# Kernel optimization log

Hardware: AMD Instinct MI355X
Metric: run time of the kernel (lower is better)

Reference implementation:

```python
import jax, jax.numpy as jnp
import numpy as np
from jax import lax

PAD0, PAD1 = 2, 2  # kernel_size=3 -> pad = (3//2+1, (3+1)//2) = (2, 2)


def make_blur_kernel():
    k = jnp.array([1.0, 3.0, 3.0, 1.0], dtype=jnp.float32)
    k2 = k[None, :] * k[:, None]  # [4,4] binomial
    return k2 / jnp.sum(k2)


def setup_inputs() -> dict:
    key = jax.random.key(0)
    x = jax.random.normal(key, (16, 256, 128, 128), dtype=jnp.float32)
    kernel = make_blur_kernel()  # fixed (buffer) 4x4 normalized binomial filter
    return {"x": x, "kernel": kernel}


def reference(x, kernel):
    # upfirdn2d(x, k, up=1, down=1, padding=(2,2)):
    # zero-pad H and W by (2,2) each, depthwise FIR filter with the 4x4 kernel.
    # Kernel is symmetric, so correlation == convolution.
    C = x.shape[1]
    w = jnp.broadcast_to(kernel[None, None, :, :], (C, 1, 4, 4))  # depthwise OIHW
    out = lax.conv_general_dilated(
        x, w,
        window_strides=(1, 1),
        padding=((PAD0, PAD1), (PAD0, PAD1)),
        feature_group_count=C,
        dimension_numbers=("NCHW", "OIHW", "NCHW"),
    )
    # output: [16, 256, 129, 129] (H + pad0 + pad1 - 4 + 1)
    return out
```

## Files before the change

### kernel.cpp

```cpp
#include <hip/hip_runtime.h>


#define BAR() __builtin_amdgcn_s_barrier()
#define WAITV(NSTR) do {                                                     \
        asm volatile("s_waitcnt vmcnt(" NSTR ")" ::: "memory");              \
        __builtin_amdgcn_sched_barrier(0);                                   \
    } while (0)

__global__ __launch_bounds__(512, 8) void blur_fir_ring4(
    const float* __restrict__ x,
    const float* __restrict__ kern,
    float* __restrict__ out)
{
    __shared__ __align__(16) float lds[4 * 16 * 128];

    const int tid  = threadIdx.x;
    const int wv   = tid >> 6;
    const int lane = tid & 63;
    const int c    = tid >> 5;
    const int g    = tid & 31;
    const bool lv  = (g >= 1);

    const float* __restrict__ xi = x + (size_t)blockIdx.x * (128 * 128);
    float* __restrict__ oi = out + (size_t)blockIdx.x * (129 * 129);

    float w[4][4];
#pragma unroll
    for (int p = 0; p < 4; ++p)
#pragma unroll
        for (int q = 0; q < 4; ++q)
            w[p][q] = kern[4 * p + q];

#define STAGE(J) do {                                                        \
        int p0_ = 16 * (J) - 2 + 2 * wv;                                     \
        p0_ = p0_ < 0 ? 0 : (p0_ > 126 ? 126 : p0_);      \
        const float* src_ = xi + (size_t)p0_ * 128 + (lane << 2);            \
        const float* dst_ = &lds[((J) & 3) * 2048 + wv * 256];               \
        __builtin_amdgcn_global_load_lds(                                    \
            (const __attribute__((address_space(1))) unsigned int*)src_,     \
            (__attribute__((address_space(3))) unsigned int*)dst_,           \
            16, 0, 0);                                                       \
    } while (0)

#define COMPUTE(J) do {                                                      \
        float o0 = 0.f, o1 = 0.f, o2 = 0.f, o3 = 0.f;                        \
        float e0 = 0.f, e1 = 0.f, e2 = 0.f;                                  \
        _Pragma("unroll")                                                    \
        for (int p = 0; p < 4; ++p) {                                        \
            const int  k_   = c + p;                                         \
            const bool okr_ = ((unsigned)(16 * (J) - 2 + k_)) < 128u;        \
            const float* pb_ = ((k_ < 16)                                    \
                ? &lds[((J) & 3) * 2048 + k_ * 128]                          \
                : &lds[(((J) + 1) & 3) * 2048 + (k_ - 16) * 128])            \
                + 4 * g - 4;                                                 \
            float4 a_ = make_float4(0.f, 0.f, 0.f, 0.f);                     \
            float4 b_ = make_float4(0.f, 0.f, 0.f, 0.f);                     \
            if (okr_ && lv) a_ = *(const float4*)pb_;                        \
            if (okr_)       b_ = *(const float4*)(pb_ + 4);                  \
            o0 = fmaf(a_.x, w[p][0], o0);                                    \
            o1 = fmaf(a_.y, w[p][0], o1);                                    \
            o2 = fmaf(a_.z, w[p][0], o2);                                    \
            o3 = fmaf(a_.w, w[p][0], o3);                                    \
            o0 = fmaf(a_.y, w[p][1], o0);                                    \
            o1 = fmaf(a_.z, w[p][1], o1);                                    \
            o2 = fmaf(a_.w, w[p][1], o2);                                    \
            o3 = fmaf(b_.x, w[p][1], o3);                                    \
            o0 = fmaf(a_.z, w[p][2], o0);                                    \
            o1 = fmaf(a_.w, w[p][2], o1);                                    \
            o2 = fmaf(b_.x, w[p][2], o2);                                    \
            o3 = fmaf(b_.y, w[p][2], o3);                                    \
            o0 = fmaf(a_.w, w[p][3], o0);                                    \
            o1 = fmaf(b_.x, w[p][3], o1);                                    \
            o2 = fmaf(b_.y, w[p][3], o2);                                    \
            o3 = fmaf(b_.z, w[p][3], o3);                                    \
               \
            e0 = fmaf(b_.x, w[p][0], e0);                                    \
            e0 = fmaf(b_.y, w[p][1], e0);                                    \
            e0 = fmaf(b_.z, w[p][2], e0);                                    \
            e0 = fmaf(b_.w, w[p][3], e0);                                    \
            e1 = fmaf(b_.y, w[p][0], e1);                                    \
            e1 = fmaf(b_.z, w[p][1], e1);                                    \
            e1 = fmaf(b_.w, w[p][2], e1);                                    \
            e2 = fmaf(b_.z, w[p][0], e2);                                    \
            e2 = fmaf(b_.w, w[p][1], e2);                                    \
        }                                                                    \
        float* po_ = oi + (size_t)(16 * (J) + c) * 129 + 4 * g - 2;          \
        if (lv) { po_[0] = o0; po_[1] = o1; }                                \
        po_[2] = o2;                                                         \
        po_[3] = o3;                                                         \
        if (g == 31) { po_[4] = e0; po_[5] = e1; po_[6] = e2; }              \
    } while (0)

    STAGE(0); STAGE(1); STAGE(2); STAGE(3);

    WAITV("2");  BAR(); COMPUTE(0); BAR(); STAGE(4);
    WAITV("9");  BAR(); COMPUTE(1); BAR(); STAGE(5);
    WAITV("16"); BAR(); COMPUTE(2); BAR(); STAGE(6);
    WAITV("16"); BAR(); COMPUTE(3); BAR(); STAGE(7);
    WAITV("16"); BAR(); COMPUTE(4); BAR(); STAGE(8);
    WAITV("16"); BAR(); COMPUTE(5); BAR();
    WAITV("15"); BAR(); COMPUTE(6); BAR();
    WAITV("14"); BAR(); COMPUTE(7); BAR();

    if (c == 0) COMPUTE(8);

#undef STAGE
#undef COMPUTE
}

extern "C" void kernel_launch(void* const* d_in, const int* in_sizes, int n_in,
                              void* d_out, int out_size, void* d_ws, size_t ws_size,
                              hipStream_t stream) {
    const float* x    = (const float*)d_in[0];
    const float* kern = (const float*)d_in[1];
    float* out        = (float*)d_out;

    dim3 grid(4096), block(512);
    hipLaunchKernelGGL(blur_fir_ring4, grid, block, 0, stream, x, kern, out);
}
```

Baseline: 116.0 us.

## Give each wave a private LDS ring to drop block barriers; split right-edge columns into separate kernel

Each wave now stages and consumes only its own 16-row band through a private 6-slot LDS ring. This removes the block-wide s_barrier calls between stages, using only vmcnt/lgkmcnt waits. Each thread computes two output rows per iteration, reusing the loaded input rows for both. The three rightmost output columns, formerly handled by a divergent g==31 branch, move to a second small kernel, which adds a launch and some redundant global reads. LDS use grows and the occupancy hint drops from 8 to 6 blocks.

```diff
diff --git a/kernel.cpp b/kernel.cpp
--- a/kernel.cpp
+++ b/kernel.cpp
@@ -1,25 +1,28 @@
 #include <hip/hip_runtime.h>
 
 
-#define BAR() __builtin_amdgcn_s_barrier()
 #define WAITV(NSTR) do {                                                     \
         asm volatile("s_waitcnt vmcnt(" NSTR ")" ::: "memory");              \
         __builtin_amdgcn_sched_barrier(0);                                   \
     } while (0)
+#define WAITL() do {                                                         \
+        asm volatile("s_waitcnt lgkmcnt(0)" ::: "memory");                   \
+        __builtin_amdgcn_sched_barrier(0);                                   \
+    } while (0)
 
-__global__ __launch_bounds__(512, 8) void blur_fir_ring4(
+__global__ __launch_bounds__(512, 6) void blur_main(
     const float* __restrict__ x,
     const float* __restrict__ kern,
     float* __restrict__ out)
 {
-    __shared__ __align__(16) float lds[4 * 16 * 128];
+    __shared__ __align__(16) float lds[8 * 6 * 256];
 
     const int tid  = threadIdx.x;
     const int wv   = tid >> 6;
     const int lane = tid & 63;
-    const int c    = tid >> 5;
-    const int g    = tid & 31;
-    const bool lv  = (g >= 1);
+    const int h    = lane >> 5;
+    const int g    = lane & 31;
+    const int r0   = wv << 4;
 
     const float* __restrict__ xi = x + (size_t)blockIdx.x * (128 * 128);
     float* __restrict__ oi = out + (size_t)blockIdx.x * (129 * 129);
@@ -31,81 +34,136 @@
         for (int q = 0; q < 4; ++q)
             w[p][q] = kern[4 * p + q];
 
-#define STAGE(J) do {                                                        \
-        int p0_ = 16 * (J) - 2 + 2 * wv;                                     \
-        p0_ = p0_ < 0 ? 0 : (p0_ > 126 ? 126 : p0_);      \
+    float* const wbase = &lds[wv * 1536];
+
+#define STAGEPAIR(Q) do {                                                    \
+        int p0_ = r0 - 2 + 2 * (Q);                                          \
+        p0_ = p0_ < 0 ? 0 : (p0_ > 126 ? 126 : p0_);                         \
         const float* src_ = xi + (size_t)p0_ * 128 + (lane << 2);            \
-        const float* dst_ = &lds[((J) & 3) * 2048 + wv * 256];               \
+        const float* dst_ = wbase + ((Q) % 6) * 256;                         \
         __builtin_amdgcn_global_load_lds(                                    \
             (const __attribute__((address_space(1))) unsigned int*)src_,     \
             (__attribute__((address_space(3))) unsigned int*)dst_,           \
             16, 0, 0);                                                       \
     } while (0)
 
-#define COMPUTE(J) do {                                                      \
-        float o0 = 0.f, o1 = 0.f, o2 = 0.f, o3 = 0.f;                        \
-        float e0 = 0.f, e1 = 0.f, e2 = 0.f;                                  \
-        _Pragma("unroll")                                                    \
-        for (int p = 0; p < 4; ++p) {                                        \
-            const int  k_   = c + p;                                         \
-            const bool okr_ = ((unsigned)(16 * (J) - 2 + k_)) < 128u;        \
-            const float* pb_ = ((k_ < 16)                                    \
-                ? &lds[((J) & 3) * 2048 + k_ * 128]                          \
-                : &lds[(((J) + 1) & 3) * 2048 + (k_ - 16) * 128])            \
-                + 4 * g - 4;                                                 \
-            float4 a_ = make_float4(0.f, 0.f, 0.f, 0.f);                     \
-            float4 b_ = make_float4(0.f, 0.f, 0.f, 0.f);                     \
-            if (okr_ && lv) a_ = *(const float4*)pb_;                        \
-            if (okr_)       b_ = *(const float4*)(pb_ + 4);                  \
-            o0 = fmaf(a_.x, w[p][0], o0);                                    \
-            o1 = fmaf(a_.y, w[p][0], o1);                                    \
-            o2 = fmaf(a_.z, w[p][0], o2);                                    \
-            o3 = fmaf(a_.w, w[p][0], o3);                                    \
-            o0 = fmaf(a_.y, w[p][1], o0);                                    \
-            o1 = fmaf(a_.z, w[p][1], o1);                                    \
-            o2 = fmaf(a_.w, w[p][1], o2);                                    \
-            o3 = fmaf(b_.x, w[p][1], o3);                                    \
-            o0 = fmaf(a_.z, w[p][2], o0);                                    \
-            o1 = fmaf(a_.w, w[p][2], o1);                                    \
-            o2 = fmaf(b_.x, w[p][2], o2);                                    \
-            o3 = fmaf(b_.y, w[p][2], o3);                                    \
-            o0 = fmaf(a_.w, w[p][3], o0);                                    \
-            o1 = fmaf(b_.x, w[p][3], o1);                                    \
-            o2 = fmaf(b_.y, w[p][3], o2);                                    \
-            o3 = fmaf(b_.z, w[p][3], o3);                                    \
-               \
-            e0 = fmaf(b_.x, w[p][0], e0);                                    \
-            e0 = fmaf(b_.y, w[p][1], e0);                                    \
-            e0 = fmaf(b_.z, w[p][2], e0);                                    \
-            e0 = fmaf(b_.w, w[p][3], e0);                                    \
-            e1 = fmaf(b_.y, w[p][0], e1);                                    \
-            e1 = fmaf(b_.z, w[p][1], e1);                                    \
-            e1 = fmaf(b_.w, w[p][2], e1);                                    \
-            e2 = fmaf(b_.z, w[p][0], e2);                                    \
-            e2 = fmaf(b_.w, w[p][1], e2);                                    \
-        }                                                                    \
-        float* po_ = oi + (size_t)(16 * (J) + c) * 129 + 4 * g - 2;          \
-        if (lv) { po_[0] = o0; po_[1] = o1; }                                \
-        po_[2] = o2;                                                         \
-        po_[3] = o3;                                                         \
-        if (g == 31) { po_[4] = e0; po_[5] = e1; po_[6] = e2; }              \
+#define FMA4(O0, O1, O2, O3, AV, BV, P) do {                                 \
+        O0 = fmaf(AV.x, w[P][0], O0);                                        \
+        O0 = fmaf(AV.y, w[P][1], O0);                                        \
+        O0 = fmaf(AV.z, w[P][2], O0);                                        \
+        O0 = fmaf(AV.w, w[P][3], O0);                                        \
+        O1 = fmaf(AV.y, w[P][0], O1);                                        \
+        O1 = fmaf(AV.z, w[P][1], O1);                                        \
+        O1 = fmaf(AV.w, w[P][2], O1);                                        \
+        O1 = fmaf(BV.x, w[P][3], O1);                                        \
+        O2 = fmaf(AV.z, w[P][0], O2);                                        \
+        O2 = fmaf(AV.w, w[P][1], O2);                                        \
+        O2 = fmaf(BV.x, w[P][2], O2);                                        \
+        O2 = fmaf(BV.y, w[P][3], O2);                                        \
+        O3 = fmaf(AV.w, w[P][0], O3);                                        \
+        O3 = fmaf(BV.x, w[P][1], O3);                                        \
+        O3 = fmaf(BV.y, w[P][2], O3);                                        \
+        O3 = fmaf(BV.z, w[P][3], O3);                                        \
     } while (0)
 
-    STAGE(0); STAGE(1); STAGE(2); STAGE(3);
+#define CITER(I) do {                                                        \
+        float oA0=0.f, oA1=0.f, oA2=0.f, oA3=0.f;                            \
+        float oB0=0.f, oB1=0.f, oB2=0.f, oB3=0.f;                            \
+        _Pragma("unroll")                                                    \
+        for (int m = 0; m < 5; ++m) {                                        \
+            const int K = (2 * (I) + (m >> 1)) % 6;                          \
+            int sl = K + h; sl = (sl >= 6) ? (sl - 6) : sl;                  \
+            const int rowv = r0 - 2 + 4 * (I) + 2 * h + m;                   \
+            const bool okr = (unsigned)rowv < 128u;                          \
+            const float* pa = wbase + sl * 256 + (m & 1) * 128 + 4 * g;      \
+            float4 av = make_float4(0.f, 0.f, 0.f, 0.f);                     \
+            float4 bv = make_float4(0.f, 0.f, 0.f, 0.f);                     \
+            if (okr && g) av = *(const float4*)(pa - 4);                     \
+            if (okr)      bv = *(const float4*)pa;                           \
+            if (m < 4) FMA4(oA0, oA1, oA2, oA3, av, bv, m);                  \
+            if (m > 0) FMA4(oB0, oB1, oB2, oB3, av, bv, (m - 1));            \
+        }                                                                    \
+        float* po = oi + (size_t)(r0 + 4 * (I) + 2 * h) * 129 + 4 * g - 2;   \
+        if (g) { po[0] = oA0; po[1] = oA1; }                                 \
+        po[2] = oA2; po[3] = oA3;                                            \
+        po += 129;                                                           \
+        if (g) { po[0] = oB0; po[1] = oB1; }                                 \
+        po[2] = oB2; po[3] = oB3;                                            \
+    } while (0)
 
-    WAITV("2");  BAR(); COMPUTE(0); BAR(); STAGE(4);
-    WAITV("9");  BAR(); COMPUTE(1); BAR(); STAGE(5);
-    WAITV("16"); BAR(); COMPUTE(2); BAR(); STAGE(6);
-    WAITV("16"); BAR(); COMPUTE(3); BAR(); STAGE(7);
-    WAITV("16"); BAR(); COMPUTE(4); BAR(); STAGE(8);
-    WAITV("16"); BAR(); COMPUTE(5); BAR();
-    WAITV("15"); BAR(); COMPUTE(6); BAR();
-    WAITV("14"); BAR(); COMPUTE(7); BAR();
+    STAGEPAIR(0); STAGEPAIR(1); STAGEPAIR(2);
+    STAGEPAIR(3); STAGEPAIR(4); STAGEPAIR(5);
 
-    if (c == 0) COMPUTE(8);
+    WAITV("2");
+    CITER(0);
+    WAITL(); STAGEPAIR(6); STAGEPAIR(7);
+    WAITV("10");
+    CITER(1);
+    WAITL(); STAGEPAIR(8); STAGEPAIR(9);
+    WAITV("10");
+    CITER(2);
+    WAITV("8");
+    CITER(3);
 
-#undef STAGE
-#undef COMPUTE
+    if (wv == 7) {
+        float oT0=0.f, oT1=0.f, oT2=0.f, oT3=0.f;
+        const float* pa = wbase + 2 * 256 + 4 * g;
+        float4 av = make_float4(0.f, 0.f, 0.f, 0.f);
+        float4 bv;
+        if (g) av = *(const float4*)(pa - 4);
+        bv = *(const float4*)pa;
+        FMA4(oT0, oT1, oT2, oT3, av, bv, 0);
+        av = make_float4(0.f, 0.f, 0.f, 0.f);
+        if (g) av = *(const float4*)(pa + 128 - 4);
+        bv = *(const float4*)(pa + 128);
+        FMA4(oT0, oT1, oT2, oT3, av, bv, 1);
+        if (!h) {
+            float* po = oi + (size_t)128 * 129 + 4 * g - 2;
+            if (g) { po[0] = oT0; po[1] = oT1; }
+            po[2] = oT2; po[3] = oT3;
+        }
+    }
+
+#undef STAGEPAIR
+#undef FMA4
+#undef CITER
+}
+
+__global__ __launch_bounds__(256) void blur_edge(
+    const float* __restrict__ x,
+    const float* __restrict__ kern,
+    float* __restrict__ out)
+{
+    const int id  = blockIdx.x * 256 + threadIdx.x;
+    const int img = id / 129;
+    const int r   = id - img * 129;
+
+    float w[4][4];
+#pragma unroll
+    for (int p = 0; p < 4; ++p)
+#pragma unroll
+        for (int q = 0; q < 4; ++q)
+            w[p][q] = kern[4 * p + q];
+
+    const float* xi = x + (size_t)img * (128 * 128) + 124;
+    float e0 = 0.f, e1 = 0.f, e2 = 0.f;
+#pragma unroll
+    for (int p = 0; p < 4; ++p) {
+        const int rr = r - 2 + p;
+        float4 v = make_float4(0.f, 0.f, 0.f, 0.f);
+        if ((unsigned)rr < 128u) v = *(const float4*)(xi + (size_t)rr * 128);
+        e0 = fmaf(v.x, w[p][0], e0);
+        e0 = fmaf(v.y, w[p][1], e0);
+        e0 = fmaf(v.z, w[p][2], e0);
+        e0 = fmaf(v.w, w[p][3], e0);
+        e1 = fmaf(v.y, w[p][0], e1);
+        e1 = fmaf(v.z, w[p][1], e1);
+        e1 = fmaf(v.w, w[p][2], e1);
+        e2 = fmaf(v.z, w[p][0], e2);
+        e2 = fmaf(v.w, w[p][1], e2);
+    }
+    float* po = out + (size_t)img * (129 * 129) + (size_t)r * 129 + 126;
+    po[0] = e0; po[1] = e1; po[2] = e2;
 }
 
 extern "C" void kernel_launch(void* const* d_in, const int* in_sizes, int n_in,
@@ -115,6 +173,6 @@
     const float* kern = (const float*)d_in[1];
     float* out        = (float*)d_out;
 
-    dim3 grid(4096), block(512);
-    hipLaunchKernelGGL(blur_fir_ring4, grid, block, 0, stream, x, kern, out);
+    hipLaunchKernelGGL(blur_main, dim3(4096), dim3(512), 0, stream, x, kern, out);
+    hipLaunchKernelGGL(blur_edge, dim3(2064), dim3(256), 0, stream, x, kern, out);
 }
```

Measured after the change: 169.1 us. 1.46x slower.
